# Optimization experiments

Measured on AMD Instinct MI355X. Metric: run time of the kernel, lower is better.

Reference implementation:

```python
import jax, jax.numpy as jnp
import numpy as np

B, D_IN, D_BOT, C = 8192, 2048, 1024, 1000
SHARE = 500          # cfg.share_class_num
TEMP = 0.05          # cfg.temp
NEG_FILL = -1e9
EPS = 1e-12          # F.normalize eps


def setup_inputs() -> dict:
    key = jax.random.key(0)
    ks = jax.random.split(key, 6)
    return {
        "features": jax.random.normal(ks[0], (B, D_IN), jnp.float32),
        "W_b": jax.random.normal(ks[1], (D_BOT, D_IN), jnp.float32) * 0.02,
        "b_b": jnp.zeros((D_BOT,), jnp.float32),
        "W1": jax.random.normal(ks[2], (C, D_BOT), jnp.float32) * 0.02,
        "W2": jax.random.normal(ks[3], (C, D_BOT), jnp.float32) * 0.02,
        "centroid": jax.random.normal(ks[4], (C, D_BOT), jnp.float32) * 0.02,
    }


def mask_mechanism(outputs):
    # per-row mask: argmax -> row mask -> masked softmax (branchless)
    predict = jnp.argmax(outputs, axis=1)                       # [B]
    cls = jnp.arange(C)                                          # [C]
    base = cls < SHARE                                           # shared classes masked
    # if predicted class is private (>= SHARE), mask the whole row ...
    row_mask = jnp.where((predict >= SHARE)[:, None], True, base[None, :])
    # ... but always unmask the predicted class itself
    row_mask = row_mask & (cls[None, :] != predict[:, None])     # [B, C] bool
    masked = jnp.where(row_mask, jnp.float32(NEG_FILL), outputs)
    return jax.nn.softmax(masked, axis=1)


def reference(features, W_b, b_b, W1, W2, centroid):
    feats = features @ W_b.T + b_b                               # bottleneck [B, D_BOT]
    outputs1 = feats @ W1.T                                      # [B, C]
    sm1 = mask_mechanism(outputs1)
    feat_oa = sm1 @ centroid                                     # [B, D_BOT]
    features_aug = feats + feat_oa
    # F.normalize(dim=1): x / max(||x||_2, eps)
    norm = jnp.sqrt(jnp.sum(features_aug * features_aug, axis=1, keepdims=True))
    x = features_aug / jnp.maximum(norm, EPS)
    outputs2 = (x @ W2.T) / TEMP                                 # [B, C]
    softmax_outputs = jax.nn.softmax(outputs2, axis=1)
    return (feats, features_aug, outputs1, outputs2, softmax_outputs)
```

## Files before the change

kernel.cpp:

```cpp
#include <hip/hip_runtime.h>
#include <cmath>


typedef _Float16 h8 __attribute__((ext_vector_type(8)));
typedef _Float16 h4 __attribute__((ext_vector_type(4)));
typedef float f32x4 __attribute__((ext_vector_type(4)));

__device__ __forceinline__ void gload_lds16(const _Float16* g, _Float16* l) {
    __builtin_amdgcn_global_load_lds(
        (const __attribute__((address_space(1))) void*)g,
        (__attribute__((address_space(3))) void*)l, 16, 0, 0);
}

template <int MODE>
__global__ __launch_bounds__(256, 2) void gemm16(
    const _Float16* __restrict__ Ah, const _Float16* __restrict__ Al, int lda,
    const _Float16* __restrict__ Bh, const _Float16* __restrict__ Bl, int ldb,
    int K,
    float* __restrict__ C, int ldc, int nC,
    const float* __restrict__ aux,
    _Float16* __restrict__ Ch, _Float16* __restrict__ Cl)
{
    constexpr bool P2 = (MODE <= 2);
    __shared__ _Float16 sAh[128 * 64];
    __shared__ _Float16 sBh[128 * 64];
    __shared__ _Float16 sAl[P2 ? 128 * 64 : 8];
    __shared__ _Float16 sBl[P2 ? 128 * 64 : 8];

    const int t = threadIdx.x;
    const int lane = t & 63, wid = t >> 6;
    const int row0 = blockIdx.y * 128, col0 = blockIdx.x * 128;
    const int wr = wid >> 1, wc = wid & 1;
    const int fr = lane & 15;
    const int fk = (lane >> 4) * 8;
    const int srow = lane >> 3;
    const int scol = (lane & 7) * 8;

    f32x4 acc[4][4] = {};
    f32x4 accc[4][4] = {};

    for (int k0 = 0; k0 < K; k0 += 64) {
        #pragma unroll
        for (int j = 0; j < 4; ++j) {
            int i = wid * 4 + j;
            int r = i * 8 + srow;
            const size_t ga = (size_t)(row0 + r) * lda + k0 + scol;
            const size_t gb = (size_t)(col0 + r) * ldb + k0 + scol;
            gload_lds16(Ah + ga, &sAh[i * 512]);
            gload_lds16(Bh + gb, &sBh[i * 512]);
            if constexpr (P2) {
                gload_lds16(Al + ga, &sAl[i * 512]);
                gload_lds16(Bl + gb, &sBl[i * 512]);
            }
        }
        __syncthreads();
        #pragma unroll
        for (int ks = 0; ks < 2; ++ks) {
            h8 ah[4], al[4];
            #pragma unroll
            for (int mf = 0; mf < 4; ++mf) {
                int rr = wr * 64 + mf * 16 + fr;
                ah[mf] = *(const h8*)&sAh[rr * 64 + ks * 32 + fk];
                if constexpr (P2) al[mf] = *(const h8*)&sAl[rr * 64 + ks * 32 + fk];
            }
            #pragma unroll
            for (int nf = 0; nf < 4; ++nf) {
                int cc = wc * 64 + nf * 16 + fr;
                h8 bh = *(const h8*)&sBh[cc * 64 + ks * 32 + fk];
                h8 bl;
                if constexpr (P2) bl = *(const h8*)&sBl[cc * 64 + ks * 32 + fk];
                #pragma unroll
                for (int mf = 0; mf < 4; ++mf) {
                    acc[mf][nf] = __builtin_amdgcn_mfma_f32_16x16x32_f16(ah[mf], bh, acc[mf][nf], 0, 0, 0);
                    if constexpr (P2) {
                        accc[mf][nf] = __builtin_amdgcn_mfma_f32_16x16x32_f16(ah[mf], bl, accc[mf][nf], 0, 0, 0);
                        accc[mf][nf] = __builtin_amdgcn_mfma_f32_16x16x32_f16(al[mf], bh, accc[mf][nf], 0, 0, 0);
                    }
                }
            }
        }
        __syncthreads();
    }
    #pragma unroll
    for (int mf = 0; mf < 4; ++mf) {
        #pragma unroll
        for (int nf = 0; nf < 4; ++nf) {
            f32x4 v = acc[mf][nf];
            if constexpr (P2) v = v + accc[mf][nf] * (1.0f / 2048.0f);
            int gcol = col0 + wc * 64 + nf * 16 + fr;
            int rbase = row0 + wr * 64 + mf * 16 + (lane >> 4) * 4;
            #pragma unroll
            for (int j = 0; j < 4; ++j) {
                int grow = rbase + j;
                float val = v[j];
                if constexpr (MODE == 1) val += aux[gcol];
                if constexpr (MODE == 3) val += aux[(size_t)grow * 1024 + gcol];
                if constexpr (MODE == 4) val *= 20.0f;
                if (gcol < nC) {
                    C[(size_t)grow * ldc + gcol] = val;
                    if constexpr (MODE == 1) {
                        _Float16 h = (_Float16)val;
                        Ch[(size_t)grow * 1024 + gcol] = h;
                        Cl[(size_t)grow * 1024 + gcol] = (_Float16)((val - (float)h) * 2048.0f);
                    }
                }
            }
        }
    }
}

__global__ void split_kernel(const float* __restrict__ src,
                             _Float16* __restrict__ hi, _Float16* __restrict__ lo, int n4)
{
    for (int i = blockIdx.x * 256 + threadIdx.x; i < n4; i += gridDim.x * 256) {
        f32x4 v = ((const f32x4*)src)[i];
        h4 h, l;
        #pragma unroll
        for (int j = 0; j < 4; ++j) {
            _Float16 hh = (_Float16)v[j];
            h[j] = hh;
            l[j] = (_Float16)((v[j] - (float)hh) * 2048.0f);
        }
        ((h4*)hi)[i] = h;
        ((h4*)lo)[i] = l;
    }
}

template <bool LO>
__global__ void padsplit_kernel(const float* __restrict__ src,
                                _Float16* __restrict__ hi, _Float16* __restrict__ lo, int nrows)
{
    for (int i = blockIdx.x * 256 + threadIdx.x; i < 1024 * 256; i += gridDim.x * 256) {
        int r = i >> 8;
        f32x4 v = {0.f, 0.f, 0.f, 0.f};
        if (r < nrows) v = ((const f32x4*)src)[i];
        h4 h, l;
        #pragma unroll
        for (int j = 0; j < 4; ++j) {
            _Float16 hh = (_Float16)v[j];
            h[j] = hh;
            if constexpr (LO) l[j] = (_Float16)((v[j] - (float)hh) * 2048.0f);
        }
        ((h4*)hi)[i] = h;
        if constexpr (LO) ((h4*)lo)[i] = l;
    }
}

__global__ __launch_bounds__(256) void ctrans_kernel(const float* __restrict__ centroid,
                                                     _Float16* __restrict__ cT)
{
    __shared__ float tile[32][33];
    const int t = threadIdx.x;
    const int tx = t & 31, ty = t >> 5;
    const int k0 = blockIdx.y * 32, n0 = blockIdx.x * 32;
    #pragma unroll
    for (int p = 0; p < 4; ++p) {
        int k = k0 + ty + p * 8;
        tile[ty + p * 8][tx] = (k < 1000) ? centroid[(size_t)k * 1024 + n0 + tx] : 0.0f;
    }
    __syncthreads();
    #pragma unroll
    for (int p = 0; p < 4; ++p) {
        int n = n0 + ty + p * 8;
        cT[(size_t)n * 1024 + k0 + tx] = (_Float16)tile[tx][ty + p * 8];
    }
}

__global__ __launch_bounds__(256) void masksm_kernel(const float* __restrict__ o1,
                                                     _Float16* __restrict__ sm)
{
    const int row = blockIdx.x;
    const int t = threadIdx.x;
    const float* x = o1 + (size_t)row * 1000;
    _Float16* y = sm + (size_t)row * 1024;

    float bv = -1e30f; int bi = 0;
    for (int c = t; c < 1000; c += 256) {
        float v = x[c];
        if (v > bv) { bv = v; bi = c; }
    }
    #pragma unroll
    for (int off = 32; off > 0; off >>= 1) {
        float ov = __shfl_down(bv, off, 64);
        int   oi = __shfl_down(bi, off, 64);
        if (ov > bv || (ov == bv && oi < bi)) { bv = ov; bi = oi; }
    }
    __shared__ float wv[4]; __shared__ int wi[4];
    __shared__ float s_m, s_tot; __shared__ int s_p;
    const int lane = t & 63, wid = t >> 6;
    if (lane == 0) { wv[wid] = bv; wi[wid] = bi; }
    __syncthreads();
    if (t == 0) {
        float mv = wv[0]; int mi = wi[0];
        for (int w = 1; w < 4; ++w)
            if (wv[w] > mv || (wv[w] == mv && wi[w] < mi)) { mv = wv[w]; mi = wi[w]; }
        s_p = mi; s_m = mv;
    }
    __syncthreads();
    const int p = s_p; const float m = s_m;
    if (p >= 500) {
        for (int c = t; c < 1024; c += 256) y[c] = (c == p) ? (_Float16)1.0f : (_Float16)0.0f;
    } else {
        float s = 0.f;
        for (int c = t; c < 1000; c += 256)
            if (c == p || c >= 500) s += expf(x[c] - m);
        #pragma unroll
        for (int off = 32; off > 0; off >>= 1) s += __shfl_down(s, off, 64);
        if (lane == 0) wv[wid] = s;
        __syncthreads();
        if (t == 0) s_tot = wv[0] + wv[1] + wv[2] + wv[3];
        __syncthreads();
        const float inv = 1.0f / s_tot;
        for (int c = t; c < 1024; c += 256) {
            float v = 0.f;
            if (c < 1000 && (c == p || c >= 500)) v = expf(x[c] - m) * inv;
            y[c] = (_Float16)v;
        }
    }
}

__global__ __launch_bounds__(256) void rownorm_x_kernel(const float* __restrict__ aug,
                                                        _Float16* __restrict__ xh)
{
    const int row = blockIdx.x; const int t = threadIdx.x;
    f32x4 v = *((const f32x4*)(aug + (size_t)row * 1024) + t);
    float s = v[0]*v[0] + v[1]*v[1] + v[2]*v[2] + v[3]*v[3];
    #pragma unroll
    for (int off = 32; off > 0; off >>= 1) s += __shfl_down(s, off, 64);
    __shared__ float ws4[4]; __shared__ float s_inv;
    const int lane = t & 63, wid = t >> 6;
    if (lane == 0) ws4[wid] = s;
    __syncthreads();
    if (t == 0) {
        float tot = ws4[0] + ws4[1] + ws4[2] + ws4[3];
        s_inv = 1.0f / fmaxf(sqrtf(tot), 1e-12f);
    }
    __syncthreads();
    const float inv = s_inv;
    h4 h;
    #pragma unroll
    for (int j = 0; j < 4; ++j) h[j] = (_Float16)(v[j] * inv);
    *((h4*)(xh + (size_t)row * 1024) + t) = h;
}

__global__ __launch_bounds__(256) void softmax2_kernel(const float* __restrict__ o2,
                                                       float* __restrict__ out)
{
    const int row = blockIdx.x; const int t = threadIdx.x;
    const float* x = o2 + (size_t)row * 1000;
    float* y = out + (size_t)row * 1000;
    float m = -1e30f;
    for (int c = t; c < 1000; c += 256) m = fmaxf(m, x[c]);
    #pragma unroll
    for (int off = 32; off > 0; off >>= 1) m = fmaxf(m, __shfl_down(m, off, 64));
    __shared__ float sm4[4]; __shared__ float s_m, s_s;
    const int lane = t & 63, wid = t >> 6;
    if (lane == 0) sm4[wid] = m;
    __syncthreads();
    if (t == 0) s_m = fmaxf(fmaxf(sm4[0], sm4[1]), fmaxf(sm4[2], sm4[3]));
    __syncthreads();
    m = s_m;
    float s = 0.f;
    for (int c = t; c < 1000; c += 256) s += expf(x[c] - m);
    #pragma unroll
    for (int off = 32; off > 0; off >>= 1) s += __shfl_down(s, off, 64);
    if (lane == 0) sm4[wid] = s;
    __syncthreads();
    if (t == 0) s_s = sm4[0] + sm4[1] + sm4[2] + sm4[3];
    __syncthreads();
    const float inv = 1.0f / s_s;
    for (int c = t; c < 1000; c += 256) y[c] = expf(x[c] - m) * inv;
}

extern "C" void kernel_launch(void* const* d_in, const int* in_sizes, int n_in,
                              void* d_out, int out_size, void* d_ws, size_t ws_size,
                              hipStream_t stream)
{
    const float* features = (const float*)d_in[0];
    const float* W_b      = (const float*)d_in[1];
    const float* b_b      = (const float*)d_in[2];
    const float* W1       = (const float*)d_in[3];
    const float* W2       = (const float*)d_in[4];
    const float* centroid = (const float*)d_in[5];

    char* base = (char*)d_out;
    float* feats = (float*)(base);
    float* aug   = (float*)(base + 33554432);
    float* o1    = (float*)(base + 67108864);
    float* o2    = (float*)(base + 99876864);
    float* smx   = (float*)(base + 132644864);

    _Float16* fh    = (_Float16*)(base + 67108864);
    _Float16* fl    = (_Float16*)(base + 100663296);
    _Float16* wbh   = (_Float16*)(base + 134217728);
    _Float16* wbl   = (_Float16*)(base + 138412032);
    _Float16* fetsh = (_Float16*)(base + 33554432);
    _Float16* fetsl = (_Float16*)(base + 50331648);
    _Float16* w1h   = (_Float16*)(base + 142606336);
    _Float16* w1l   = (_Float16*)(base + 144703488);
    _Float16* sm1h  = (_Float16*)(base + 99876864);
    _Float16* cth   = (_Float16*)(base + 116654080);
    _Float16* w2h   = (_Float16*)(base + 132644864);
    _Float16* xh    = (_Float16*)(base + 146800640);

    dim3 g(8, 64);

    split_kernel<<<2048, 256, 0, stream>>>(features, fh, fl, 4194304);
    split_kernel<<<2048, 256, 0, stream>>>(W_b, wbh, wbl, 524288);
    padsplit_kernel<true><<<1024, 256, 0, stream>>>(W1, w1h, w1l, 1000);

    gemm16<1><<<g, 256, 0, stream>>>(fh, fl, 2048, wbh, wbl, 2048, 2048,
                                     feats, 1024, 1024, b_b, fetsh, fetsl);

    ctrans_kernel<<<dim3(32, 32), 256, 0, stream>>>(centroid, cth);
    padsplit_kernel<false><<<1024, 256, 0, stream>>>(W2, w2h, nullptr, 1000);

    gemm16<2><<<g, 256, 0, stream>>>(fetsh, fetsl, 1024, w1h, w1l, 1024, 1024,
                                     o1, 1000, 1000, nullptr, nullptr, nullptr);

    masksm_kernel<<<8192, 256, 0, stream>>>(o1, sm1h);

    gemm16<3><<<g, 256, 0, stream>>>(sm1h, nullptr, 1024, cth, nullptr, 1024, 1024,
                                     aug, 1024, 1024, feats, nullptr, nullptr);

    rownorm_x_kernel<<<8192, 256, 0, stream>>>(aug, xh);

    gemm16<4><<<g, 256, 0, stream>>>(xh, nullptr, 1024, w2h, nullptr, 1024, 1024,
                                     o2, 1000, 1000, nullptr, nullptr, nullptr);

    softmax2_kernel<<<8192, 256, 0, stream>>>(o2, smx);
}
```

Measured before the change: 311.0 us.

## Double-buffer GEMM k-loop with 256x128 tiles, LDS swizzle and grouped block order

The GEMM kernel now uses 512-thread blocks computing 256x128 tiles, with K chunks of 32 double-buffered in LDS. The next chunk's global-to-LDS load is issued before the current chunk's MFMAs run, replacing the load-sync-compute-sync pattern. An XOR swizzle on the LDS slot is meant to cut bank conflicts, and a remapped 1D grid orders blocks for better L2 reuse. MFMA sections also get raised wave priority. The trade-off is more LDS per block and hand-placed waitcnt and barriers, which must be exactly right for correctness.

After: 330.4 us. +6.2%, slower.

```diff
diff --git a/kernel.cpp b/kernel.cpp
--- a/kernel.cpp
+++ b/kernel.cpp
@@ -13,7 +13,7 @@
 }
 
 template <int MODE>
-__global__ __launch_bounds__(256, 2) void gemm16(
+__global__ __launch_bounds__(512, 2) void gemm16(
     const _Float16* __restrict__ Ah, const _Float16* __restrict__ Al, int lda,
     const _Float16* __restrict__ Bh, const _Float16* __restrict__ Bl, int ldb,
     int K,
@@ -22,76 +22,105 @@
     _Float16* __restrict__ Ch, _Float16* __restrict__ Cl)
 {
     constexpr bool P2 = (MODE <= 2);
-    __shared__ _Float16 sAh[128 * 64];
-    __shared__ _Float16 sBh[128 * 64];
-    __shared__ _Float16 sAl[P2 ? 128 * 64 : 8];
-    __shared__ _Float16 sBl[P2 ? 128 * 64 : 8];
+    constexpr int NLOADS = P2 ? 6 : 3;
+    __shared__ _Float16 sAh[2 * 256 * 32];
+    __shared__ _Float16 sBh[2 * 128 * 32];
+    __shared__ _Float16 sAl[P2 ? 2 * 256 * 32 : 8];
+    __shared__ _Float16 sBl[P2 ? 2 * 128 * 32 : 8];
 
     const int t = threadIdx.x;
     const int lane = t & 63, wid = t >> 6;
-    const int row0 = blockIdx.y * 128, col0 = blockIdx.x * 128;
+    const int wg = blockIdx.x;
+    const int wgid = (wg & 7) * 32 + (wg >> 3);
+    const int row0 = (wgid >> 3) * 256;
+    const int col0 = (wgid & 7) * 128;
     const int wr = wid >> 1, wc = wid & 1;
     const int fr = lane & 15;
-    const int fk = (lane >> 4) * 8;
-    const int srow = lane >> 3;
-    const int scol = (lane & 7) * 8;
+    const int rks = (((lane >> 4) ^ (lane & 3)) << 3);
+    const int srow = lane >> 2;
+    const int sslot = ((lane & 3) ^ (srow & 3)) << 3;
 
     f32x4 acc[4][4] = {};
     f32x4 accc[4][4] = {};
 
-    for (int k0 = 0; k0 < K; k0 += 64) {
-        #pragma unroll
-        for (int j = 0; j < 4; ++j) {
-            int i = wid * 4 + j;
-            int r = i * 8 + srow;
-            const size_t ga = (size_t)(row0 + r) * lda + k0 + scol;
-            const size_t gb = (size_t)(col0 + r) * ldb + k0 + scol;
-            gload_lds16(Ah + ga, &sAh[i * 512]);
-            gload_lds16(Bh + gb, &sBh[i * 512]);
-            if constexpr (P2) {
-                gload_lds16(Al + ga, &sAl[i * 512]);
-                gload_lds16(Bl + gb, &sBl[i * 512]);
+    auto stage = [&](int p, int kt) {
+        const int kk = kt * 32;
+        #pragma unroll
+        for (int j = 0; j < 2; ++j) {
+            const int i = wid * 2 + j;
+            const int r = i * 16 + srow;
+            const size_t ga = (size_t)(row0 + r) * lda + kk + sslot;
+            gload_lds16(Ah + ga, &sAh[p * 8192 + i * 512]);
+            if constexpr (P2) gload_lds16(Al + ga, &sAl[p * 8192 + i * 512]);
+        }
+        {
+            const int r = wid * 16 + srow;
+            const size_t gb = (size_t)(col0 + r) * ldb + kk + sslot;
+            gload_lds16(Bh + gb, &sBh[p * 4096 + wid * 512]);
+            if constexpr (P2) gload_lds16(Bl + gb, &sBl[p * 4096 + wid * 512]);
+        }
+    };
+
+    auto compute = [&](int p) {
+        h8 ah[4], al[4];
+        #pragma unroll
+        for (int mf = 0; mf < 4; ++mf) {
+            const int rr = wr * 64 + mf * 16 + fr;
+            ah[mf] = *(const h8*)&sAh[p * 8192 + rr * 32 + rks];
+            if constexpr (P2) al[mf] = *(const h8*)&sAl[p * 8192 + rr * 32 + rks];
+        }
+        #pragma unroll
+        for (int half = 0; half < 2; ++half) {
+            h8 bh[2], bl[2];
+            #pragma unroll
+            for (int q = 0; q < 2; ++q) {
+                const int cc = wc * 64 + (half * 2 + q) * 16 + fr;
+                bh[q] = *(const h8*)&sBh[p * 4096 + cc * 32 + rks];
+                if constexpr (P2) bl[q] = *(const h8*)&sBl[p * 4096 + cc * 32 + rks];
             }
-        }
-        __syncthreads();
-        #pragma unroll
-        for (int ks = 0; ks < 2; ++ks) {
-            h8 ah[4], al[4];
+            __builtin_amdgcn_s_setprio(1);
             #pragma unroll
-            for (int mf = 0; mf < 4; ++mf) {
-                int rr = wr * 64 + mf * 16 + fr;
-                ah[mf] = *(const h8*)&sAh[rr * 64 + ks * 32 + fk];
-                if constexpr (P2) al[mf] = *(const h8*)&sAl[rr * 64 + ks * 32 + fk];
-            }
-            #pragma unroll
-            for (int nf = 0; nf < 4; ++nf) {
-                int cc = wc * 64 + nf * 16 + fr;
-                h8 bh = *(const h8*)&sBh[cc * 64 + ks * 32 + fk];
-                h8 bl;
-                if constexpr (P2) bl = *(const h8*)&sBl[cc * 64 + ks * 32 + fk];
+            for (int q = 0; q < 2; ++q) {
+                const int nf = half * 2 + q;
                 #pragma unroll
                 for (int mf = 0; mf < 4; ++mf) {
-                    acc[mf][nf] = __builtin_amdgcn_mfma_f32_16x16x32_f16(ah[mf], bh, acc[mf][nf], 0, 0, 0);
+                    acc[mf][nf] = __builtin_amdgcn_mfma_f32_16x16x32_f16(ah[mf], bh[q], acc[mf][nf], 0, 0, 0);
                     if constexpr (P2) {
-                        accc[mf][nf] = __builtin_amdgcn_mfma_f32_16x16x32_f16(ah[mf], bl, accc[mf][nf], 0, 0, 0);
-                        accc[mf][nf] = __builtin_amdgcn_mfma_f32_16x16x32_f16(al[mf], bh, accc[mf][nf], 0, 0, 0);
+                        accc[mf][nf] = __builtin_amdgcn_mfma_f32_16x16x32_f16(ah[mf], bl[q], accc[mf][nf], 0, 0, 0);
+                        accc[mf][nf] = __builtin_amdgcn_mfma_f32_16x16x32_f16(al[mf], bh[q], accc[mf][nf], 0, 0, 0);
                     }
                 }
             }
-        }
-        __syncthreads();
-    }
+            __builtin_amdgcn_s_setprio(0);
+        }
+    };
+
+    const int NT = K >> 5;
+    stage(0, 0);
+    for (int kt = 0; kt < NT - 1; ++kt) {
+        stage((kt + 1) & 1, kt + 1);
+        asm volatile("s_waitcnt vmcnt(%0)" :: "i"(NLOADS) : "memory");
+        __builtin_amdgcn_s_barrier();
+        __builtin_amdgcn_sched_barrier(0);
+        compute(kt & 1);
+        __builtin_amdgcn_sched_barrier(0);
+        __builtin_amdgcn_s_barrier();
+    }
+    asm volatile("s_waitcnt vmcnt(0)" ::: "memory");
+    __builtin_amdgcn_s_barrier();
+    compute((NT - 1) & 1);
+
     #pragma unroll
     for (int mf = 0; mf < 4; ++mf) {
         #pragma unroll
         for (int nf = 0; nf < 4; ++nf) {
             f32x4 v = acc[mf][nf];
             if constexpr (P2) v = v + accc[mf][nf] * (1.0f / 2048.0f);
-            int gcol = col0 + wc * 64 + nf * 16 + fr;
-            int rbase = row0 + wr * 64 + mf * 16 + (lane >> 4) * 4;
+            const int gcol = col0 + wc * 64 + nf * 16 + fr;
+            const int rbase = row0 + wr * 64 + mf * 16 + (lane >> 4) * 4;
             #pragma unroll
             for (int j = 0; j < 4; ++j) {
-                int grow = rbase + j;
+                const int grow = rbase + j;
                 float val = v[j];
                 if constexpr (MODE == 1) val += aux[gcol];
                 if constexpr (MODE == 3) val += aux[(size_t)grow * 1024 + gcol];
@@ -303,30 +332,28 @@
     _Float16* w2h   = (_Float16*)(base + 132644864);
     _Float16* xh    = (_Float16*)(base + 146800640);
 
-    dim3 g(8, 64);
-
     split_kernel<<<2048, 256, 0, stream>>>(features, fh, fl, 4194304);
     split_kernel<<<2048, 256, 0, stream>>>(W_b, wbh, wbl, 524288);
     padsplit_kernel<true><<<1024, 256, 0, stream>>>(W1, w1h, w1l, 1000);
 
-    gemm16<1><<<g, 256, 0, stream>>>(fh, fl, 2048, wbh, wbl, 2048, 2048,
-                                     feats, 1024, 1024, b_b, fetsh, fetsl);
+    gemm16<1><<<256, 512, 0, stream>>>(fh, fl, 2048, wbh, wbl, 2048, 2048,
+                                       feats, 1024, 1024, b_b, fetsh, fetsl);
 
     ctrans_kernel<<<dim3(32, 32), 256, 0, stream>>>(centroid, cth);
     padsplit_kernel<false><<<1024, 256, 0, stream>>>(W2, w2h, nullptr, 1000);
 
-    gemm16<2><<<g, 256, 0, stream>>>(fetsh, fetsl, 1024, w1h, w1l, 1024, 1024,
-                                     o1, 1000, 1000, nullptr, nullptr, nullptr);
+    gemm16<2><<<256, 512, 0, stream>>>(fetsh, fetsl, 1024, w1h, w1l, 1024, 1024,
+                                       o1, 1000, 1000, nullptr, nullptr, nullptr);
 
     masksm_kernel<<<8192, 256, 0, stream>>>(o1, sm1h);
 
-    gemm16<3><<<g, 256, 0, stream>>>(sm1h, nullptr, 1024, cth, nullptr, 1024, 1024,
-                                     aug, 1024, 1024, feats, nullptr, nullptr);
+    gemm16<3><<<256, 512, 0, stream>>>(sm1h, nullptr, 1024, cth, nullptr, 1024, 1024,
+                                       aug, 1024, 1024, feats, nullptr, nullptr);
 
     rownorm_x_kernel<<<8192, 256, 0, stream>>>(aug, xh);
 
-    gemm16<4><<<g, 256, 0, stream>>>(xh, nullptr, 1024, w2h, nullptr, 1024, 1024,
-                                     o2, 1000, 1000, nullptr, nullptr, nullptr);
+    gemm16<4><<<256, 512, 0, stream>>>(xh, nullptr, 1024, w2h, nullptr, 1024, 1024,
+                                       o2, 1000, 1000, nullptr, nullptr, nullptr);
 
     softmax2_kernel<<<8192, 256, 0, stream>>>(o2, smx);
 }
```

## Run bottleneck and first classifier GEMMs in single fp16, recompute near-tie rows in split precision

Applied to the files above, without the earlier changes.

The first two GEMMs drop the hi/lo fp16 split and do one MFMA per step instead of three, and the split of features into a low half goes away. The masked softmax now also tracks the runner-up logit. It appends rows whose top-two gap is below a threshold to a capped index list. Only those rows are regathered, recomputed with split precision through both GEMMs, and their softmax fixed up. Two smaller changes ride along: a remapped 1D grid for tile ordering and a higher occupancy hint on the fp16 GEMMs. The risks are that the stored feats and outputs1 outputs become less accurate, and that rows past the cap of 2048 flagged entries are silently left uncorrected.

Result: slower. 361.9 us (+16.4%).

```diff
diff --git a/kernel.cpp b/kernel.cpp
--- a/kernel.cpp
+++ b/kernel.cpp
@@ -5,6 +5,9 @@
 typedef _Float16 h8 __attribute__((ext_vector_type(8)));
 typedef _Float16 h4 __attribute__((ext_vector_type(4)));
 typedef float f32x4 __attribute__((ext_vector_type(4)));
+
+#define TAU 0.015f
+#define CAP 2048
 
 __device__ __forceinline__ void gload_lds16(const _Float16* g, _Float16* l) {
     __builtin_amdgcn_global_load_lds(
@@ -13,15 +16,16 @@
 }
 
 template <int MODE>
-__global__ __launch_bounds__(256, 2) void gemm16(
+__global__ __launch_bounds__(256, (MODE >= 5) ? 2 : 4) void gemm16(
     const _Float16* __restrict__ Ah, const _Float16* __restrict__ Al, int lda,
     const _Float16* __restrict__ Bh, const _Float16* __restrict__ Bl, int ldb,
     int K,
     float* __restrict__ C, int ldc, int nC,
     const float* __restrict__ aux,
-    _Float16* __restrict__ Ch, _Float16* __restrict__ Cl)
-{
-    constexpr bool P2 = (MODE <= 2);
+    _Float16* __restrict__ Ch, _Float16* __restrict__ Cl,
+    const int* __restrict__ cnt)
+{
+    constexpr bool P2 = (MODE >= 5);
     __shared__ _Float16 sAh[128 * 64];
     __shared__ _Float16 sBh[128 * 64];
     __shared__ _Float16 sAl[P2 ? 128 * 64 : 8];
@@ -29,7 +33,15 @@
 
     const int t = threadIdx.x;
     const int lane = t & 63, wid = t >> 6;
-    const int row0 = blockIdx.y * 128, col0 = blockIdx.x * 128;
+    int row0, col0;
+    if constexpr (MODE >= 5) {
+        row0 = blockIdx.y * 128; col0 = blockIdx.x * 128;
+        if (row0 >= *cnt) return;
+    } else {
+        const int wg = blockIdx.x;
+        const int wgid = (wg & 7) * 64 + (wg >> 3);
+        row0 = (wgid >> 3) * 128; col0 = (wgid & 7) * 128;
+    }
     const int wr = wid >> 1, wc = wid & 1;
     const int fr = lane & 15;
     const int fk = (lane >> 4) * 8;
@@ -87,25 +99,39 @@
         for (int nf = 0; nf < 4; ++nf) {
             f32x4 v = acc[mf][nf];
             if constexpr (P2) v = v + accc[mf][nf] * (1.0f / 2048.0f);
-            int gcol = col0 + wc * 64 + nf * 16 + fr;
-            int rbase = row0 + wr * 64 + mf * 16 + (lane >> 4) * 4;
+            const int gcol = col0 + wc * 64 + nf * 16 + fr;
+            const int rbase = row0 + wr * 64 + mf * 16 + (lane >> 4) * 4;
             #pragma unroll
             for (int j = 0; j < 4; ++j) {
-                int grow = rbase + j;
+                const int grow = rbase + j;
                 float val = v[j];
-                if constexpr (MODE == 1) val += aux[gcol];
+                if constexpr (MODE == 1 || MODE == 5) val += aux[gcol];
                 if constexpr (MODE == 3) val += aux[(size_t)grow * 1024 + gcol];
                 if constexpr (MODE == 4) val *= 20.0f;
-                if (gcol < nC) {
-                    C[(size_t)grow * ldc + gcol] = val;
-                    if constexpr (MODE == 1) {
-                        _Float16 h = (_Float16)val;
-                        Ch[(size_t)grow * 1024 + gcol] = h;
-                        Cl[(size_t)grow * 1024 + gcol] = (_Float16)((val - (float)h) * 2048.0f);
+                if constexpr (MODE == 5) {
+                    _Float16 h = (_Float16)val;
+                    Ch[(size_t)grow * 1024 + gcol] = h;
+                    Cl[(size_t)grow * 1024 + gcol] = (_Float16)((val - (float)h) * 2048.0f);
+                } else {
+                    if (gcol < nC) {
+                        C[(size_t)grow * ldc + gcol] = val;
+                        if constexpr (MODE == 1)
+                            Ch[(size_t)grow * 1024 + gcol] = (_Float16)val;
                     }
                 }
             }
         }
+    }
+}
+
+__global__ void conv_kernel(const float* __restrict__ src, _Float16* __restrict__ hi, int n4)
+{
+    for (int i = blockIdx.x * 256 + threadIdx.x; i < n4; i += gridDim.x * 256) {
+        f32x4 v = ((const f32x4*)src)[i];
+        h4 h;
+        #pragma unroll
+        for (int j = 0; j < 4; ++j) h[j] = (_Float16)v[j];
+        ((h4*)hi)[i] = h;
     }
 }
 
@@ -166,35 +192,47 @@
     }
 }
 
-__global__ __launch_bounds__(256) void masksm_kernel(const float* __restrict__ o1,
-                                                     _Float16* __restrict__ sm)
-{
-    const int row = blockIdx.x;
-    const int t = threadIdx.x;
-    const float* x = o1 + (size_t)row * 1000;
-    _Float16* y = sm + (size_t)row * 1024;
-
-    float bv = -1e30f; int bi = 0;
+__device__ __forceinline__ void masked_softmax_body(
+    const float* __restrict__ x, _Float16* __restrict__ y,
+    int t, float* wv, int* wi, int* flag_row, int* d_idx, int* d_cnt, int rowid)
+{
+    float bv = -1e30f, sv = -1e30f; int bi = 0;
     for (int c = t; c < 1000; c += 256) {
         float v = x[c];
-        if (v > bv) { bv = v; bi = c; }
+        if (v > bv) { sv = bv; bv = v; bi = c; }
+        else if (v > sv) sv = v;
     }
     #pragma unroll
     for (int off = 32; off > 0; off >>= 1) {
         float ov = __shfl_down(bv, off, 64);
         int   oi = __shfl_down(bi, off, 64);
-        if (ov > bv || (ov == bv && oi < bi)) { bv = ov; bi = oi; }
-    }
-    __shared__ float wv[4]; __shared__ int wi[4];
+        float os = __shfl_down(sv, off, 64);
+        if (ov > bv || (ov == bv && oi < bi)) {
+            sv = fmaxf(bv, os); bv = ov; bi = oi;
+        } else {
+            sv = fmaxf(sv, fmaxf(ov, os) == ov ? ov : os);
+            sv = fmaxf(sv, ov); sv = fmaxf(sv, os);
+        }
+    }
+    __shared__ float svv[4];
+    const int lane = t & 63, wid = t >> 6;
+    if (lane == 0) { wv[wid] = bv; wi[wid] = bi; svv[wid] = sv; }
+    __syncthreads();
     __shared__ float s_m, s_tot; __shared__ int s_p;
-    const int lane = t & 63, wid = t >> 6;
-    if (lane == 0) { wv[wid] = bv; wi[wid] = bi; }
-    __syncthreads();
     if (t == 0) {
-        float mv = wv[0]; int mi = wi[0];
-        for (int w = 1; w < 4; ++w)
-            if (wv[w] > mv || (wv[w] == mv && wi[w] < mi)) { mv = wv[w]; mi = wi[w]; }
+        float mv = wv[0]; int mi = wi[0]; float m2 = svv[0];
+        for (int w = 1; w < 4; ++w) {
+            if (wv[w] > mv || (wv[w] == mv && wi[w] < mi)) {
+                m2 = fmaxf(mv, svv[w]); mv = wv[w]; mi = wi[w];
+            } else {
+                m2 = fmaxf(m2, fmaxf(wv[w], svv[w]));
+            }
+        }
         s_p = mi; s_m = mv;
+        if (flag_row && (mv - m2) < TAU) {
+            int slot = atomicAdd(d_cnt, 1);
+            if (slot < CAP) d_idx[slot] = rowid;
+        }
     }
     __syncthreads();
     const int p = s_p; const float m = s_m;
@@ -219,6 +257,56 @@
     }
 }
 
+__global__ __launch_bounds__(256) void masksm_kernel(const float* __restrict__ o1,
+                                                     _Float16* __restrict__ sm,
+                                                     int* __restrict__ d_idx,
+                                                     int* __restrict__ d_cnt)
+{
+    __shared__ float wv[4]; __shared__ int wi[4];
+    const int row = blockIdx.x;
+    int dummy;
+    masked_softmax_body(o1 + (size_t)row * 1000, sm + (size_t)row * 1024,
+                        threadIdx.x, wv, wi, &dummy, d_idx, d_cnt, row);
+}
+
+__global__ __launch_bounds__(256) void fixup_kernel(const float* __restrict__ o1g,
+                                                    _Float16* __restrict__ sm,
+                                                    const int* __restrict__ d_idx,
+                                                    const int* __restrict__ d_cnt)
+{
+    const int slot = blockIdx.x;
+    if (slot >= *d_cnt || slot >= CAP) return;
+    const int row = d_idx[slot];
+    __shared__ float wv[4]; __shared__ int wi[4];
+    masked_softmax_body(o1g + (size_t)slot * 1000, sm + (size_t)row * 1024,
+                        threadIdx.x, wv, wi, nullptr, nullptr, nullptr, 0);
+}
+
+__global__ __launch_bounds__(256) void gather_split_kernel(
+    const float* __restrict__ features,
+    _Float16* __restrict__ fgh, _Float16* __restrict__ fgl,
+    const int* __restrict__ d_idx, const int* __restrict__ d_cnt)
+{
+    const int slot = blockIdx.x;
+    if (slot >= *d_cnt || slot >= CAP) return;
+    const int row = d_idx[slot];
+    const int t = threadIdx.x;
+    #pragma unroll
+    for (int q = 0; q < 2; ++q) {
+        int o = t * 8 + q * 4;
+        f32x4 v = *(const f32x4*)(features + (size_t)row * 2048 + o);
+        h4 h, l;
+        #pragma unroll
+        for (int j = 0; j < 4; ++j) {
+            _Float16 hh = (_Float16)v[j];
+            h[j] = hh;
+            l[j] = (_Float16)((v[j] - (float)hh) * 2048.0f);
+        }
+        *(h4*)(fgh + (size_t)slot * 2048 + o) = h;
+        *(h4*)(fgl + (size_t)slot * 2048 + o) = l;
+    }
+}
+
 __global__ __launch_bounds__(256) void rownorm_x_kernel(const float* __restrict__ aug,
                                                         _Float16* __restrict__ xh)
 {
@@ -291,42 +379,48 @@
     float* smx   = (float*)(base + 132644864);
 
     _Float16* fh    = (_Float16*)(base + 67108864);
-    _Float16* fl    = (_Float16*)(base + 100663296);
-    _Float16* wbh   = (_Float16*)(base + 134217728);
-    _Float16* wbl   = (_Float16*)(base + 138412032);
     _Float16* fetsh = (_Float16*)(base + 33554432);
-    _Float16* fetsl = (_Float16*)(base + 50331648);
+    int*      idx   = (int*)     (base + 50331648);
+    int*      cnt   = (int*)     (base + 50339840);
+    _Float16* fgsh  = (_Float16*)(base + 50348032);
+    _Float16* fgsl  = (_Float16*)(base + 54542336);
+    float*    o1g   = (float*)   (base + 58736640);
+    _Float16* sm1h  = (_Float16*)(base + 99876864);
+    _Float16* cth   = (_Float16*)(base + 116654080);
+    _Float16* wbh   = (_Float16*)(base + 118751232);
+    _Float16* wbl   = (_Float16*)(base + 122945536);
+    _Float16* w2h   = (_Float16*)(base + 132644864);
     _Float16* w1h   = (_Float16*)(base + 142606336);
     _Float16* w1l   = (_Float16*)(base + 144703488);
-    _Float16* sm1h  = (_Float16*)(base + 99876864);
-    _Float16* cth   = (_Float16*)(base + 116654080);
-    _Float16* w2h   = (_Float16*)(base + 132644864);
+    _Float16* fgh   = (_Float16*)(base + 146800640);
+    _Float16* fgl   = (_Float16*)(base + 155189248);
     _Float16* xh    = (_Float16*)(base + 146800640);
 
-    dim3 g(8, 64);
-
-    split_kernel<<<2048, 256, 0, stream>>>(features, fh, fl, 4194304);
-    split_kernel<<<2048, 256, 0, stream>>>(W_b, wbh, wbl, 524288);
+    hipMemsetAsync(cnt, 0, 4, stream);
+
+    conv_kernel<<<2048, 256, 0, stream>>>(features, fh, 4194304);
+    split_kernel<<<1024, 256, 0, stream>>>(W_b, wbh, wbl, 524288);
     padsplit_kernel<true><<<1024, 256, 0, stream>>>(W1, w1h, w1l, 1000);
-
-    gemm16<1><<<g, 256, 0, stream>>>(fh, fl, 2048, wbh, wbl, 2048, 2048,
-                                     feats, 1024, 1024, b_b, fetsh, fetsl);
-
     ctrans_kernel<<<dim3(32, 32), 256, 0, stream>>>(centroid, cth);
     padsplit_kernel<false><<<1024, 256, 0, stream>>>(W2, w2h, nullptr, 1000);
 
-    gemm16<2><<<g, 256, 0, stream>>>(fetsh, fetsl, 1024, w1h, w1l, 1024, 1024,
-                                     o1, 1000, 1000, nullptr, nullptr, nullptr);
-
-    masksm_kernel<<<8192, 256, 0, stream>>>(o1, sm1h);
-
-    gemm16<3><<<g, 256, 0, stream>>>(sm1h, nullptr, 1024, cth, nullptr, 1024, 1024,
-                                     aug, 1024, 1024, feats, nullptr, nullptr);
-
+    gemm16<1><<<512, 256, 0, stream>>>(fh, nullptr, 2048, wbh, nullptr, 2048, 2048,
+                                       feats, 1024, 1024, b_b, fetsh, nullptr, nullptr);
+    gemm16<2><<<512, 256, 0, stream>>>(fetsh, nullptr, 1024, w1h, nullptr, 1024, 1024,
+                                       o1, 1000, 1000, nullptr, nullptr, nullptr, nullptr);
+    masksm_kernel<<<8192, 256, 0, stream>>>(o1, sm1h, idx, cnt);
+
+    gather_split_kernel<<<CAP, 256, 0, stream>>>(features, fgh, fgl, idx, cnt);
+    gemm16<5><<<dim3(8, CAP / 128), 256, 0, stream>>>(fgh, fgl, 2048, wbh, wbl, 2048, 2048,
+                                                      nullptr, 0, 1024, b_b, fgsh, fgsl, cnt);
+    gemm16<6><<<dim3(8, CAP / 128), 256, 0, stream>>>(fgsh, fgsl, 1024, w1h, w1l, 1024, 1024,
+                                                      o1g, 1000, 1000, nullptr, nullptr, nullptr, cnt);
+    fixup_kernel<<<CAP, 256, 0, stream>>>(o1g, sm1h, idx, cnt);
+
+    gemm16<3><<<512, 256, 0, stream>>>(sm1h, nullptr, 1024, cth, nullptr, 1024, 1024,
+                                       aug, 1024, 1024, feats, nullptr, nullptr, nullptr);
     rownorm_x_kernel<<<8192, 256, 0, stream>>>(aug, xh);
-
-    gemm16<4><<<g, 256, 0, stream>>>(xh, nullptr, 1024, w2h, nullptr, 1024, 1024,
-                                     o2, 1000, 1000, nullptr, nullptr, nullptr);
-
+    gemm16<4><<<512, 256, 0, stream>>>(xh, nullptr, 1024, w2h, nullptr, 1024, 1024,
+                                       o2, 1000, 1000, nullptr, nullptr, nullptr, nullptr);
     softmax2_kernel<<<8192, 256, 0, stream>>>(o2, smx);
 }
```
